# Optimization experiments

Measured on AMD Instinct MI355X. Metric: run time of the kernel, lower is better.

Reference implementation:

```python
import math
import jax, jax.numpy as jnp
import numpy as np

B, S, D, H, V = 8, 1024, 512, 8, 32000
HD = D // H


def _position_embedding(seq_len, d_model):
    pos = jnp.arange(seq_len, dtype=jnp.float32)[:, None]                 # [S,1]
    div = jnp.exp(jnp.arange(0, d_model, 2, dtype=jnp.float32) * (-math.log(10000.0) / d_model))  # [D/2]
    ang = pos * div                                                        # [S,D/2]
    # interleave sin (even cols) / cos (odd cols)
    return jnp.stack([jnp.sin(ang), jnp.cos(ang)], axis=-1).reshape(seq_len, d_model)


def _min_max_normalize(w):
    lo = jnp.min(w, axis=-1, keepdims=True)
    hi = jnp.max(w, axis=-1, keepdims=True)
    return (w - lo) / (hi - lo)


def _converable_mask(h, Wc, bc):
    bs, seq = h.shape[0], h.shape[1]
    half = seq // 2
    shift = math.ceil(seq / 2)
    width = jnp.einsum('bsd,od->bso', h, Wc)[..., 0] + bc[0]               # [B,S]
    width = _min_max_normalize(width)[..., None]                           # [B,S,1]
    origin = jnp.concatenate([jnp.linspace(1.0, 0.0, half),
                              jnp.linspace(0.0, 1.0, seq - half)])         # [S]
    origin_mask = 1.0 - jax.nn.sigmoid((origin[None, None, :] - width) * 100.0)  # [B,S,S]
    idx = (jnp.arange(seq - 1, -1, -1)[:, None] + jnp.arange(seq)[None, :]) % seq  # [S,S]
    idx = jnp.roll(idx, shift, axis=0)
    # torch.roll of a [1,S] row along dim 0 is a no-op
    cmp = idx >= jnp.arange(seq)[None, :]                                  # [S,S] bool
    move = jnp.concatenate([cmp[:shift], ~cmp[shift:]], axis=0)            # [S,S]
    gathered = jnp.take_along_axis(origin_mask, idx[None, :, :], axis=2)   # [B,S,S]
    return gathered * move.astype(origin_mask.dtype)


def setup_inputs():
    key = jax.random.key(0)
    ks = jax.random.split(key, 9)
    s_emb = 1.0
    s_hd = 1.0 / math.sqrt(HD)
    s_d = 1.0 / math.sqrt(D)
    return {
        'x':   jax.random.randint(ks[0], (B, S), 0, V),
        'emb': jax.random.normal(ks[1], (V, D), dtype=jnp.float32) * s_emb,
        'Wq':  jax.random.normal(ks[2], (HD, HD), dtype=jnp.float32) * s_hd,
        'Wk':  jax.random.normal(ks[3], (HD, HD), dtype=jnp.float32) * s_hd,
        'Wv':  jax.random.normal(ks[4], (HD, HD), dtype=jnp.float32) * s_hd,
        'Wo':  jax.random.normal(ks[5], (D, D), dtype=jnp.float32) * s_d,
        'bo':  jnp.zeros((D,), dtype=jnp.float32),
        'Wc':  jax.random.normal(ks[6], (1, D), dtype=jnp.float32) * s_d,
        'bc':  jnp.zeros((1,), dtype=jnp.float32),
    }


def reference(x, emb, Wq, Wk, Wv, Wo, bo, Wc, bc):
    h = emb[x] + _position_embedding(S, D)[None]                           # [B,S,D]
    mask = _converable_mask(h, Wc, bc)                                     # [B,S,S]
    hh = h.reshape(B, S, H, HD)
    q = jnp.einsum('bshd,od->bsho', hh, Wq)
    k = jnp.einsum('bshd,od->bsho', hh, Wk)
    v = jnp.einsum('bshd,od->bsho', hh, Wv)
    energy = jnp.einsum('bqhd,bkhd->bhqk', q, k)                           # [B,H,S,S]
    # mask [B,S,S] broadcasts as [1,B,S,S]; valid because B == H (as in original)
    energy = energy * mask
    attn = jax.nn.softmax(energy / math.sqrt(D), axis=3)
    out = jnp.einsum('bhqk,bkhd->bqhd', attn, v).reshape(B, S, D)
    out = out @ Wo.T + bo
    return (out, mask)
```

## Files before the change

kernel.cpp:

```cpp
#include <hip/hip_runtime.h>
#include <hip/hip_bf16.h>
#include <math.h>

#define Bn 8
#define Sn 1024
#define Dn 512
#define Hn 8
#define HDn 64

typedef __bf16 bf16x8 __attribute__((ext_vector_type(8)));
typedef __bf16 bf16x4 __attribute__((ext_vector_type(4)));
typedef float  f32x4  __attribute__((ext_vector_type(4)));

__global__ void k_embed(const int* __restrict__ x, const float* __restrict__ emb,
                        float* __restrict__ h) {
    const int total = Bn * Sn * Dn;
    for (int i = blockIdx.x * blockDim.x + threadIdx.x; i < total; i += gridDim.x * blockDim.x) {
        int d = i & (Dn - 1);
        int bs = i >> 9;
        int s = bs & (Sn - 1);
        int tok = x[bs];
        float f = __expf((float)(d & ~1) * (-9.210340371976184f / 512.0f));
        float ang = (float)s * f;
        float pe = (d & 1) ? __cosf(ang) : __sinf(ang);
        h[i] = emb[(size_t)tok * Dn + d] + pe;
    }
}

__global__ void k_width(const float* __restrict__ h, const float* __restrict__ Wc,
                        const float* __restrict__ bc, float* __restrict__ width) {
    int row = blockIdx.x * 4 + (threadIdx.x >> 6);
    int lane = threadIdx.x & 63;
    const float* hr = h + (size_t)row * Dn;
    float acc = 0.f;
    for (int i = lane; i < Dn; i += 64) acc += hr[i] * Wc[i];
    for (int off = 32; off > 0; off >>= 1) acc += __shfl_down(acc, off);
    if (lane == 0) width[row] = acc + bc[0];
}

__global__ void k_minmax(const float* __restrict__ width, float* __restrict__ lo,
                         float* __restrict__ hi) {
    int b = blockIdx.x;
    __shared__ float smin[256], smax[256];
    float mn = 1e30f, mx = -1e30f;
    for (int s = threadIdx.x; s < Sn; s += 256) {
        float v = width[b * Sn + s];
        mn = fminf(mn, v);
        mx = fmaxf(mx, v);
    }
    smin[threadIdx.x] = mn; smax[threadIdx.x] = mx;
    __syncthreads();
    for (int off = 128; off; off >>= 1) {
        if (threadIdx.x < off) {
            smin[threadIdx.x] = fminf(smin[threadIdx.x], smin[threadIdx.x + off]);
            smax[threadIdx.x] = fmaxf(smax[threadIdx.x], smax[threadIdx.x + off]);
        }
        __syncthreads();
    }
    if (threadIdx.x == 0) { lo[b] = smin[0]; hi[b] = smax[0]; }
}

__global__ void k_mask(const float* __restrict__ width, const float* __restrict__ lo,
                       const float* __restrict__ hi, float* __restrict__ mask_out) {
    int bs = blockIdx.x;
    int b = bs >> 10;
    int s = bs & (Sn - 1);
    float wn = (width[bs] - lo[b]) / (hi[b] - lo[b]);
    for (int t = threadIdx.x; t < Sn; t += 256) {
        int it = (t - s + 511) & (Sn - 1);
        float origin = (it < 512) ? (1.0f - (float)it * (1.0f / 511.0f))
                                  : ((float)(it - 512) * (1.0f / 511.0f));
        float z = (origin - wn) * 100.0f;
        float om;
        if (z >= 0.0f) { float e = __expf(-z); om = e / (1.0f + e); }
        else           { float e = __expf(z);  om = 1.0f / (1.0f + e); }
        bool cmpv = (it >= t);
        bool mv = (s < 512) ? cmpv : !cmpv;
        mask_out[(size_t)bs * Sn + t] = mv ? om : 0.0f;
    }
}

__global__ void k_qkv(const float* __restrict__ h, const float* __restrict__ Wq,
                      const float* __restrict__ Wk, const float* __restrict__ Wv,
                      __bf16* __restrict__ q, __bf16* __restrict__ k, __bf16* __restrict__ vt) {
    __shared__ float Hs[8][Dn];
    __shared__ float WqS[HDn][HDn + 1];
    __shared__ float WkS[HDn][HDn + 1];
    __shared__ float WvS[HDn][HDn + 1];
    int t = threadIdx.x;
    int bs0 = blockIdx.x * 8;
    for (int i = t; i < HDn * HDn; i += 512) {
        int o = i >> 6, d = i & 63;
        WqS[d][o] = Wq[i]; WkS[d][o] = Wk[i]; WvS[d][o] = Wv[i];
    }
    for (int i = t; i < 8 * Dn; i += 512) Hs[i >> 9][i & 511] = h[(size_t)bs0 * Dn + i];
    __syncthreads();
    int head = t >> 6, o = t & 63;
    float aq[8] = {}, ak[8] = {}, av[8] = {};
    for (int d = 0; d < HDn; ++d) {
        float wq = WqS[d][o], wk = WkS[d][o], wv = WvS[d][o];
        #pragma unroll
        for (int tt = 0; tt < 8; ++tt) {
            float hv = Hs[tt][head * HDn + d];
            aq[tt] += hv * wq; ak[tt] += hv * wk; av[tt] += hv * wv;
        }
    }
    int b = bs0 >> 10, s0 = bs0 & (Sn - 1);
    int bh = b * Hn + head;
    __bf16 vloc[8];
    #pragma unroll
    for (int tt = 0; tt < 8; ++tt) {
        size_t oidx = ((size_t)bh * Sn + s0 + tt) * HDn + o;
        q[oidx] = (__bf16)aq[tt];
        k[oidx] = (__bf16)ak[tt];
        vloc[tt] = (__bf16)av[tt];
    }
    *(bf16x8*)&vt[((size_t)bh * HDn + o) * Sn + s0] = *(bf16x8*)vloc;
}

__global__ __launch_bounds__(256) void k_attn(
        const __bf16* __restrict__ q, const __bf16* __restrict__ k,
        const __bf16* __restrict__ vt, const float* __restrict__ maskf,
        __bf16* __restrict__ ao) {
    const float SCALE = 0.04419417382415922f;
    __shared__ __align__(16) __bf16 Qs[64][72];
    __shared__ __align__(16) __bf16 Ks[64][72];
    __shared__ __align__(16) __bf16 Vt[64][72];
    __shared__ __align__(16) __bf16 Ps[64][72];
    int blk = blockIdx.x;
    int qt = blk & 15;
    int bh = blk >> 4;
    int hh = bh & (Hn - 1);
    int b = bh >> 3;
    int q0 = qt * 64;
    int t = threadIdx.x;
    int w = t >> 6, lane = t & 63, quad = lane >> 4, li = lane & 15;

    const __bf16* qbase  = q  + ((size_t)bh * Sn + q0) * HDn;
    const __bf16* kbase  = k  + (size_t)bh * Sn * HDn;
    const __bf16* vtbase = vt + (size_t)bh * HDn * Sn;
    const float*  mbase  = maskf + ((size_t)hh * Sn + q0) * Sn;

    #pragma unroll
    for (int it = 0; it < 2; ++it) {
        int e = (it * 256 + t) * 8; int r = e >> 6, c = e & 63;
        *(bf16x8*)&Qs[r][c] = *(const bf16x8*)&qbase[e];
    }

    f32x4 O[4];
    #pragma unroll
    for (int n = 0; n < 4; ++n) O[n] = (f32x4){0.f, 0.f, 0.f, 0.f};
    float m_[4] = {-1e30f, -1e30f, -1e30f, -1e30f};
    float l_[4] = {0.f, 0.f, 0.f, 0.f};

    for (int k0 = 0; k0 < Sn; k0 += 64) {
        if (k0) __syncthreads();
        #pragma unroll
        for (int it = 0; it < 2; ++it) {
            int e = (it * 256 + t) * 8; int r = e >> 6, c = e & 63;
            *(bf16x8*)&Ks[r][c] = *(const bf16x8*)&kbase[(size_t)k0 * HDn + e];
            *(bf16x8*)&Vt[r][c] = *(const bf16x8*)&vtbase[(size_t)r * Sn + k0 + c];
        }
        __syncthreads();

        bf16x8 A0 = *(const bf16x8*)&Qs[w * 16 + li][quad * 8];
        bf16x8 A1 = *(const bf16x8*)&Qs[w * 16 + li][32 + quad * 8];
        f32x4 Sf[4];
        #pragma unroll
        for (int n = 0; n < 4; ++n) {
            f32x4 acc = (f32x4){0.f, 0.f, 0.f, 0.f};
            bf16x8 B0 = *(const bf16x8*)&Ks[n * 16 + li][quad * 8];
            acc = __builtin_amdgcn_mfma_f32_16x16x32_bf16(A0, B0, acc, 0, 0, 0);
            bf16x8 B1 = *(const bf16x8*)&Ks[n * 16 + li][32 + quad * 8];
            acc = __builtin_amdgcn_mfma_f32_16x16x32_bf16(A1, B1, acc, 0, 0, 0);
            Sf[n] = acc;
        }
        #pragma unroll
        for (int n = 0; n < 4; ++n)
            #pragma unroll
            for (int r = 0; r < 4; ++r)
                Sf[n][r] *= mbase[(size_t)(w * 16 + quad * 4 + r) * Sn + k0 + n * 16 + li] * SCALE;

        float mx[4];
        #pragma unroll
        for (int r = 0; r < 4; ++r)
            mx[r] = fmaxf(fmaxf(Sf[0][r], Sf[1][r]), fmaxf(Sf[2][r], Sf[3][r]));
        #pragma unroll
        for (int off = 1; off < 16; off <<= 1)
            #pragma unroll
            for (int r = 0; r < 4; ++r) mx[r] = fmaxf(mx[r], __shfl_xor(mx[r], off));
        float al[4], rs[4] = {0.f, 0.f, 0.f, 0.f};
        #pragma unroll
        for (int r = 0; r < 4; ++r) {
            float mn = fmaxf(m_[r], mx[r]);
            al[r] = __expf(m_[r] - mn);
            m_[r] = mn;
        }
        float p[4][4];
        #pragma unroll
        for (int n = 0; n < 4; ++n)
            #pragma unroll
            for (int r = 0; r < 4; ++r) {
                p[n][r] = __expf(Sf[n][r] - m_[r]);
                rs[r] += p[n][r];
            }
        #pragma unroll
        for (int off = 1; off < 16; off <<= 1)
            #pragma unroll
            for (int r = 0; r < 4; ++r) rs[r] += __shfl_xor(rs[r], off);
        #pragma unroll
        for (int r = 0; r < 4; ++r) l_[r] = l_[r] * al[r] + rs[r];
        #pragma unroll
        for (int n = 0; n < 4; ++n)
            #pragma unroll
            for (int r = 0; r < 4; ++r) O[n][r] *= al[r];

        #pragma unroll
        for (int n = 0; n < 4; ++n)
            #pragma unroll
            for (int r = 0; r < 4; ++r)
                Ps[w * 16 + quad * 4 + r][n * 16 + li] = (__bf16)p[n][r];

        #pragma unroll
        for (int kc = 0; kc < 2; ++kc) {
            bf16x8 Ap = *(const bf16x8*)&Ps[w * 16 + li][kc * 32 + quad * 8];
            #pragma unroll
            for (int n = 0; n < 4; ++n) {
                bf16x8 Bv = *(const bf16x8*)&Vt[n * 16 + li][kc * 32 + quad * 8];
                O[n] = __builtin_amdgcn_mfma_f32_16x16x32_bf16(Ap, Bv, O[n], 0, 0, 0);
            }
        }
    }

    float inv[4];
    #pragma unroll
    for (int r = 0; r < 4; ++r) inv[r] = 1.0f / l_[r];
    #pragma unroll
    for (int n = 0; n < 4; ++n)
        #pragma unroll
        for (int r = 0; r < 4; ++r)
            ao[((size_t)b * Sn + q0 + w * 16 + quad * 4 + r) * Dn + hh * HDn + n * 16 + li]
                = (__bf16)(O[n][r] * inv[r]);
}

__global__ __launch_bounds__(256) void k_proj(
        const __bf16* __restrict__ ao, const float* __restrict__ Wo,
        const float* __restrict__ bo, float* __restrict__ out) {
    __shared__ __align__(16) __bf16 As[64][72];
    __shared__ __align__(16) __bf16 Bs[64][72];
    int bm = blockIdx.x >> 3;
    int bn = blockIdx.x & 7;
    int m0 = bm * 64, n0 = bn * 64;
    int t = threadIdx.x;
    int w = t >> 6, lane = t & 63, quad = lane >> 4, li = lane & 15;

    f32x4 O[4];
    #pragma unroll
    for (int n = 0; n < 4; ++n) O[n] = (f32x4){0.f, 0.f, 0.f, 0.f};

    for (int k0 = 0; k0 < Dn; k0 += 64) {
        if (k0) __syncthreads();
        #pragma unroll
        for (int it = 0; it < 2; ++it) {
            int e = (it * 256 + t) * 8; int r = e >> 6, c = e & 63;
            *(bf16x8*)&As[r][c] = *(const bf16x8*)&ao[(size_t)(m0 + r) * Dn + k0 + c];
        }
        #pragma unroll
        for (int it = 0; it < 4; ++it) {
            int e = (it * 256 + t) * 4; int r = e >> 6, c = e & 63;
            float4 wv = *(const float4*)&Wo[(size_t)(n0 + r) * Dn + k0 + c];
            bf16x4 bv = { (__bf16)wv.x, (__bf16)wv.y, (__bf16)wv.z, (__bf16)wv.w };
            *(bf16x4*)&Bs[r][c] = bv;
        }
        __syncthreads();

        bf16x8 A0 = *(const bf16x8*)&As[w * 16 + li][quad * 8];
        bf16x8 A1 = *(const bf16x8*)&As[w * 16 + li][32 + quad * 8];
        #pragma unroll
        for (int n = 0; n < 4; ++n) {
            bf16x8 B0 = *(const bf16x8*)&Bs[n * 16 + li][quad * 8];
            O[n] = __builtin_amdgcn_mfma_f32_16x16x32_bf16(A0, B0, O[n], 0, 0, 0);
            bf16x8 B1 = *(const bf16x8*)&Bs[n * 16 + li][32 + quad * 8];
            O[n] = __builtin_amdgcn_mfma_f32_16x16x32_bf16(A1, B1, O[n], 0, 0, 0);
        }
    }

    #pragma unroll
    for (int n = 0; n < 4; ++n) {
        float bias = bo[n0 + n * 16 + li];
        #pragma unroll
        for (int r = 0; r < 4; ++r)
            out[(size_t)(m0 + w * 16 + quad * 4 + r) * Dn + n0 + n * 16 + li] = O[n][r] + bias;
    }
}

extern "C" void kernel_launch(void* const* d_in, const int* in_sizes, int n_in,
                              void* d_out, int out_size, void* d_ws, size_t ws_size,
                              hipStream_t stream) {
    const int*   x   = (const int*)d_in[0];
    const float* emb = (const float*)d_in[1];
    const float* Wq  = (const float*)d_in[2];
    const float* Wk  = (const float*)d_in[3];
    const float* Wv  = (const float*)d_in[4];
    const float* Wo  = (const float*)d_in[5];
    const float* bo  = (const float*)d_in[6];
    const float* Wc  = (const float*)d_in[7];
    const float* bc  = (const float*)d_in[8];

    float* ws    = (float*)d_ws;
    float* h     = ws;
    float* width = h + (size_t)Bn * Sn * Dn;
    float* lo    = width + Bn * Sn;
    float* hi    = lo + Bn;
    __bf16* qb   = (__bf16*)(hi + Bn);
    __bf16* kb   = qb + (size_t)Bn * Sn * Dn;
    __bf16* vtb  = kb + (size_t)Bn * Sn * Dn;
    __bf16* ao   = (__bf16*)h;

    float* out      = (float*)d_out;
    float* mask_out = out + (size_t)Bn * Sn * Dn;

    k_embed<<<4096, 256, 0, stream>>>(x, emb, h);
    k_width<<<(Bn * Sn) / 4, 256, 0, stream>>>(h, Wc, bc, width);
    k_minmax<<<Bn, 256, 0, stream>>>(width, lo, hi);
    k_mask<<<Bn * Sn, 256, 0, stream>>>(width, lo, hi, mask_out);
    k_qkv<<<(Bn * Sn) / 8, 512, 0, stream>>>(h, Wq, Wk, Wv, qb, kb, vtb);
    k_attn<<<Bn * Hn * (Sn / 64), 256, 0, stream>>>(qb, kb, vtb, mask_out, ao);
    k_proj<<<(Bn * Sn / 64) * (Dn / 64), 256, 0, stream>>>(ao, Wo, bo, out);
}
```

Baseline: 255.2 us.

## Recompute mask inside attention and move QKV projection onto MFMA

The attention kernel no longer reads the 32 MB float mask from global memory. It rebuilds each mask value on the fly from a per-row normalized width, which k_mask now also writes out. The QKV projection is rewritten as a bf16 MFMA GEMM over 64-row tiles, with V transposed through shared memory, and the Q fragments are hoisted out of the key loop. The mask index offset also changes from 511 to 1535, which gives the same value mod 1024. The cost is extra exp work per score element and bf16 rounding of h in the projection.

```diff
diff --git a/kernel.cpp b/kernel.cpp
--- a/kernel.cpp
+++ b/kernel.cpp
@@ -61,13 +61,15 @@
 }
 
 __global__ void k_mask(const float* __restrict__ width, const float* __restrict__ lo,
-                       const float* __restrict__ hi, float* __restrict__ mask_out) {
+                       const float* __restrict__ hi, float* __restrict__ mask_out,
+                       float* __restrict__ wn_out) {
     int bs = blockIdx.x;
     int b = bs >> 10;
     int s = bs & (Sn - 1);
     float wn = (width[bs] - lo[b]) / (hi[b] - lo[b]);
+    if (threadIdx.x == 0) wn_out[bs] = wn;
     for (int t = threadIdx.x; t < Sn; t += 256) {
-        int it = (t - s + 511) & (Sn - 1);
+        int it = (t - s + 1535) & (Sn - 1);
         float origin = (it < 512) ? (1.0f - (float)it * (1.0f / 511.0f))
                                   : ((float)(it - 512) * (1.0f / 511.0f));
         float z = (origin - wn) * 100.0f;
@@ -80,47 +82,88 @@
     }
 }
 
-__global__ void k_qkv(const float* __restrict__ h, const float* __restrict__ Wq,
-                      const float* __restrict__ Wk, const float* __restrict__ Wv,
-                      __bf16* __restrict__ q, __bf16* __restrict__ k, __bf16* __restrict__ vt) {
-    __shared__ float Hs[8][Dn];
-    __shared__ float WqS[HDn][HDn + 1];
-    __shared__ float WkS[HDn][HDn + 1];
-    __shared__ float WvS[HDn][HDn + 1];
+__global__ __launch_bounds__(256) void k_qkv(
+        const float* __restrict__ h, const float* __restrict__ Wq,
+        const float* __restrict__ Wk, const float* __restrict__ Wv,
+        __bf16* __restrict__ q, __bf16* __restrict__ k, __bf16* __restrict__ vt) {
+    __shared__ __align__(16) __bf16 Xs[64][72];
+    __shared__ __align__(16) __bf16 WqS[64][72];
+    __shared__ __align__(16) __bf16 WkS[64][72];
+    __shared__ __align__(16) __bf16 WvS[64][72];
     int t = threadIdx.x;
-    int bs0 = blockIdx.x * 8;
-    for (int i = t; i < HDn * HDn; i += 512) {
-        int o = i >> 6, d = i & 63;
-        WqS[d][o] = Wq[i]; WkS[d][o] = Wk[i]; WvS[d][o] = Wv[i];
-    }
-    for (int i = t; i < 8 * Dn; i += 512) Hs[i >> 9][i & 511] = h[(size_t)bs0 * Dn + i];
-    __syncthreads();
-    int head = t >> 6, o = t & 63;
-    float aq[8] = {}, ak[8] = {}, av[8] = {};
-    for (int d = 0; d < HDn; ++d) {
-        float wq = WqS[d][o], wk = WkS[d][o], wv = WvS[d][o];
-        #pragma unroll
-        for (int tt = 0; tt < 8; ++tt) {
-            float hv = Hs[tt][head * HDn + d];
-            aq[tt] += hv * wq; ak[tt] += hv * wk; av[tt] += hv * wv;
-        }
-    }
-    int b = bs0 >> 10, s0 = bs0 & (Sn - 1);
-    int bh = b * Hn + head;
-    __bf16 vloc[8];
-    #pragma unroll
-    for (int tt = 0; tt < 8; ++tt) {
-        size_t oidx = ((size_t)bh * Sn + s0 + tt) * HDn + o;
-        q[oidx] = (__bf16)aq[tt];
-        k[oidx] = (__bf16)ak[tt];
-        vloc[tt] = (__bf16)av[tt];
-    }
-    *(bf16x8*)&vt[((size_t)bh * HDn + o) * Sn + s0] = *(bf16x8*)vloc;
+    int m0 = blockIdx.x * 64;
+    int w = t >> 6, lane = t & 63, quad = lane >> 4, li = lane & 15;
+
+    #pragma unroll
+    for (int it = 0; it < 4; ++it) {
+        int e = (it * 256 + t) * 4; int r = e >> 6, c = e & 63;
+        float4 xv = *(const float4*)&h[(size_t)(m0 + r) * 64 + c];
+        *(bf16x4*)&Xs[r][c]  = (bf16x4){(__bf16)xv.x, (__bf16)xv.y, (__bf16)xv.z, (__bf16)xv.w};
+        float4 qv = *(const float4*)&Wq[e];
+        *(bf16x4*)&WqS[r][c] = (bf16x4){(__bf16)qv.x, (__bf16)qv.y, (__bf16)qv.z, (__bf16)qv.w};
+        float4 kv = *(const float4*)&Wk[e];
+        *(bf16x4*)&WkS[r][c] = (bf16x4){(__bf16)kv.x, (__bf16)kv.y, (__bf16)kv.z, (__bf16)kv.w};
+        float4 vv = *(const float4*)&Wv[e];
+        *(bf16x4*)&WvS[r][c] = (bf16x4){(__bf16)vv.x, (__bf16)vv.y, (__bf16)vv.z, (__bf16)vv.w};
+    }
+    __syncthreads();
+
+    bf16x8 A0 = *(const bf16x8*)&Xs[w * 16 + li][quad * 8];
+    bf16x8 A1 = *(const bf16x8*)&Xs[w * 16 + li][32 + quad * 8];
+    f32x4 aq[4], ak[4], av[4];
+    #pragma unroll
+    for (int n = 0; n < 4; ++n) {
+        aq[n] = (f32x4){0.f,0.f,0.f,0.f}; ak[n] = aq[n]; av[n] = aq[n];
+        bf16x8 Bq0 = *(const bf16x8*)&WqS[n * 16 + li][quad * 8];
+        bf16x8 Bq1 = *(const bf16x8*)&WqS[n * 16 + li][32 + quad * 8];
+        aq[n] = __builtin_amdgcn_mfma_f32_16x16x32_bf16(A0, Bq0, aq[n], 0, 0, 0);
+        aq[n] = __builtin_amdgcn_mfma_f32_16x16x32_bf16(A1, Bq1, aq[n], 0, 0, 0);
+        bf16x8 Bk0 = *(const bf16x8*)&WkS[n * 16 + li][quad * 8];
+        bf16x8 Bk1 = *(const bf16x8*)&WkS[n * 16 + li][32 + quad * 8];
+        ak[n] = __builtin_amdgcn_mfma_f32_16x16x32_bf16(A0, Bk0, ak[n], 0, 0, 0);
+        ak[n] = __builtin_amdgcn_mfma_f32_16x16x32_bf16(A1, Bk1, ak[n], 0, 0, 0);
+        bf16x8 Bv0 = *(const bf16x8*)&WvS[n * 16 + li][quad * 8];
+        bf16x8 Bv1 = *(const bf16x8*)&WvS[n * 16 + li][32 + quad * 8];
+        av[n] = __builtin_amdgcn_mfma_f32_16x16x32_bf16(A0, Bv0, av[n], 0, 0, 0);
+        av[n] = __builtin_amdgcn_mfma_f32_16x16x32_bf16(A1, Bv1, av[n], 0, 0, 0);
+    }
+
+    #pragma unroll
+    for (int n = 0; n < 4; ++n)
+        #pragma unroll
+        for (int r = 0; r < 4; ++r) {
+            int Rg = m0 + w * 16 + quad * 4 + r;
+            int bsI = Rg >> 3, head = Rg & 7;
+            int b = bsI >> 10, s = bsI & (Sn - 1);
+            size_t oidx = (((size_t)(b * Hn + head)) * Sn + s) * HDn + n * 16 + li;
+            q[oidx] = (__bf16)aq[n][r];
+            k[oidx] = (__bf16)ak[n][r];
+        }
+
+    __bf16 (*Vs)[72] = WqS;
+    __syncthreads();
+    #pragma unroll
+    for (int n = 0; n < 4; ++n)
+        #pragma unroll
+        for (int r = 0; r < 4; ++r)
+            Vs[w * 16 + quad * 4 + r][n * 16 + li] = (__bf16)av[n][r];
+    __syncthreads();
+    int bs0 = m0 >> 3;
+    int b = bs0 >> 10, s0l = bs0 & (Sn - 1);
+    #pragma unroll
+    for (int i = 0; i < 2; ++i) {
+        int p = t + 256 * i;
+        int head = p >> 6, o = p & 63;
+        __bf16 tmp[8];
+        #pragma unroll
+        for (int j = 0; j < 8; ++j) tmp[j] = Vs[j * 8 + head][o];
+        *(bf16x8*)&vt[(((size_t)(b * Hn + head)) * HDn + o) * Sn + s0l] = *(bf16x8*)tmp;
+    }
 }
 
 __global__ __launch_bounds__(256) void k_attn(
         const __bf16* __restrict__ q, const __bf16* __restrict__ k,
-        const __bf16* __restrict__ vt, const float* __restrict__ maskf,
+        const __bf16* __restrict__ vt, const float* __restrict__ wn,
         __bf16* __restrict__ ao) {
     const float SCALE = 0.04419417382415922f;
     __shared__ __align__(16) __bf16 Qs[64][72];
@@ -139,13 +182,23 @@
     const __bf16* qbase  = q  + ((size_t)bh * Sn + q0) * HDn;
     const __bf16* kbase  = k  + (size_t)bh * Sn * HDn;
     const __bf16* vtbase = vt + (size_t)bh * HDn * Sn;
-    const float*  mbase  = maskf + ((size_t)hh * Sn + q0) * Sn;
 
     #pragma unroll
     for (int it = 0; it < 2; ++it) {
         int e = (it * 256 + t) * 8; int r = e >> 6, c = e & 63;
         *(bf16x8*)&Qs[r][c] = *(const bf16x8*)&qbase[e];
     }
+
+    int qrow[4]; float wn100[4]; bool qlt[4];
+    #pragma unroll
+    for (int r = 0; r < 4; ++r) {
+        qrow[r] = q0 + w * 16 + quad * 4 + r;
+        wn100[r] = wn[hh * Sn + qrow[r]] * 100.0f;
+        qlt[r] = qrow[r] < 512;
+    }
+    __syncthreads();
+    bf16x8 A0 = *(const bf16x8*)&Qs[w * 16 + li][quad * 8];
+    bf16x8 A1 = *(const bf16x8*)&Qs[w * 16 + li][32 + quad * 8];
 
     f32x4 O[4];
     #pragma unroll
@@ -163,8 +216,6 @@
         }
         __syncthreads();
 
-        bf16x8 A0 = *(const bf16x8*)&Qs[w * 16 + li][quad * 8];
-        bf16x8 A1 = *(const bf16x8*)&Qs[w * 16 + li][32 + quad * 8];
         f32x4 Sf[4];
         #pragma unroll
         for (int n = 0; n < 4; ++n) {
@@ -175,11 +226,21 @@
             acc = __builtin_amdgcn_mfma_f32_16x16x32_bf16(A1, B1, acc, 0, 0, 0);
             Sf[n] = acc;
         }
-        #pragma unroll
-        for (int n = 0; n < 4; ++n)
-            #pragma unroll
-            for (int r = 0; r < 4; ++r)
-                Sf[n][r] *= mbase[(size_t)(w * 16 + quad * 4 + r) * Sn + k0 + n * 16 + li] * SCALE;
+
+        #pragma unroll
+        for (int n = 0; n < 4; ++n) {
+            int col = k0 + n * 16 + li;
+            #pragma unroll
+            for (int r = 0; r < 4; ++r) {
+                int it2 = (col - qrow[r] + 1535) & (Sn - 1);
+                float origin = (it2 < 512) ? fmaf((float)it2, -1.0f / 511.0f, 1.0f)
+                                           : (float)(it2 - 512) * (1.0f / 511.0f);
+                float z = fmaf(origin, 100.0f, -wn100[r]);
+                float om = __fdividef(1.0f, 1.0f + __expf(z));
+                bool mv = qlt[r] ? (it2 >= col) : (it2 < col);
+                Sf[n][r] *= (mv ? om : 0.0f) * SCALE;
+            }
+        }
 
         float mx[4];
         #pragma unroll
@@ -269,8 +330,7 @@
         for (int it = 0; it < 4; ++it) {
             int e = (it * 256 + t) * 4; int r = e >> 6, c = e & 63;
             float4 wv = *(const float4*)&Wo[(size_t)(n0 + r) * Dn + k0 + c];
-            bf16x4 bv = { (__bf16)wv.x, (__bf16)wv.y, (__bf16)wv.z, (__bf16)wv.w };
-            *(bf16x4*)&Bs[r][c] = bv;
+            *(bf16x4*)&Bs[r][c] = (bf16x4){(__bf16)wv.x, (__bf16)wv.y, (__bf16)wv.z, (__bf16)wv.w};
         }
         __syncthreads();
 
@@ -312,7 +372,8 @@
     float* width = h + (size_t)Bn * Sn * Dn;
     float* lo    = width + Bn * Sn;
     float* hi    = lo + Bn;
-    __bf16* qb   = (__bf16*)(hi + Bn);
+    float* wn    = hi + Bn;
+    __bf16* qb   = (__bf16*)(wn + Bn * Sn);
     __bf16* kb   = qb + (size_t)Bn * Sn * Dn;
     __bf16* vtb  = kb + (size_t)Bn * Sn * Dn;
     __bf16* ao   = (__bf16*)h;
@@ -323,8 +384,8 @@
     k_embed<<<4096, 256, 0, stream>>>(x, emb, h);
     k_width<<<(Bn * Sn) / 4, 256, 0, stream>>>(h, Wc, bc, width);
     k_minmax<<<Bn, 256, 0, stream>>>(width, lo, hi);
-    k_mask<<<Bn * Sn, 256, 0, stream>>>(width, lo, hi, mask_out);
-    k_qkv<<<(Bn * Sn) / 8, 512, 0, stream>>>(h, Wq, Wk, Wv, qb, kb, vtb);
-    k_attn<<<Bn * Hn * (Sn / 64), 256, 0, stream>>>(qb, kb, vtb, mask_out, ao);
+    k_mask<<<Bn * Sn, 256, 0, stream>>>(width, lo, hi, mask_out, wn);
+    k_qkv<<<(Bn * Sn * Hn) / 64, 256, 0, stream>>>(h, Wq, Wk, Wv, qb, kb, vtb);
+    k_attn<<<Bn * Hn * (Sn / 64), 256, 0, stream>>>(qb, kb, vtb, wn, ao);
     k_proj<<<(Bn * Sn / 64) * (Dn / 64), 256, 0, stream>>>(ao, Wo, bo, out);
 }
```

Measured after the change: 269.4 us. 5.6% more time.
